# Kernel optimization log

Measured on AMD Instinct MI355X. Metric: run time of the kernel, lower is better.

The kernel has to match this reference:

```python
import jax, jax.numpy as jnp
import numpy as np

B, T, C, H = 8, 1024, 1024, 16
NEG = -1000000000.0
EPS = 1e-12


def setup_inputs() -> dict:
    key = jax.random.key(0)
    ks = jax.random.split(key, 12)
    s = 0.02  # keep pre-softmax logits in a sane range
    return {
        "x": jax.random.normal(ks[0], (B, T, C), jnp.float32),
        "mask": jax.random.randint(ks[1], (B, T), 0, 2, jnp.int32),
        "Wq": jax.random.normal(ks[2], (C, C), jnp.float32) * s,
        "bq": jax.random.normal(ks[3], (C,), jnp.float32) * s,
        "Wk": jax.random.normal(ks[4], (C, C), jnp.float32) * s,
        "bk": jax.random.normal(ks[5], (C,), jnp.float32) * s,
        "Wv": jax.random.normal(ks[6], (C, C), jnp.float32) * s,
        "bv": jax.random.normal(ks[7], (C,), jnp.float32) * s,
        "Wp": jax.random.normal(ks[8], (C, C), jnp.float32) * s,
        "bp": jax.random.normal(ks[9], (C,), jnp.float32) * s,
        "ln_w": jnp.ones((C,), jnp.float32),
        "ln_b": jnp.zeros((C,), jnp.float32),
    }


def reference(x, mask, Wq, bq, Wk, bk, Wv, bv, Wp, bp, ln_w, ln_b):
    Bx, Tx, Cx = x.shape
    hd = Cx // H
    # torch nn.Linear: y = x @ W.T + b
    def lin(inp, W, b):
        return inp @ W.T + b

    def split_heads(t):  # [B,T,C] -> [B,H,T,hd]
        return t.reshape(Bx, Tx, H, hd).transpose(0, 2, 1, 3)

    q = split_heads(lin(x, Wq, bq))
    k = split_heads(lin(x, Wk, bk))
    v = split_heads(lin(x, Wv, bv))

    att = jnp.einsum("bhqd,bhkd->bhqk", q, k) * (1.0 / jnp.sqrt(jnp.float32(hd)))
    # mask [B,T] masks key positions; broadcast to [B,1,1,T]
    att = jnp.where(mask[:, None, None, :] == 0, NEG, att)
    # stable softmax (manual max-subtract, matching original)
    att = jax.nn.softmax(att, axis=-1)
    # dropout prob 0.0 -> identity (eval-mode faithful)
    y = jnp.einsum("bhqk,bhkd->bhqd", att, v)
    y = y.transpose(0, 2, 1, 3).reshape(Bx, Tx, Cx)
    y = lin(y, Wp, bp)
    # residual + LayerNorm(eps=1e-12)
    z = y + x
    mu = jnp.mean(z, axis=-1, keepdims=True)
    var = jnp.mean(jnp.square(z - mu), axis=-1, keepdims=True)
    out = (z - mu) * jax.lax.rsqrt(var + EPS) * ln_w + ln_b
    return out
```

## Files before the change

kernel.cpp:

```cpp
#include <hip/hip_runtime.h>
#include <stdint.h>

#define B_ 8
#define T_ 1024
#define C_ 1024
#define H_ 16
#define HD 64
#define M_TOT (B_ * T_)

using f32x4 = __attribute__((ext_vector_type(4))) float;
using s16x8 = __attribute__((ext_vector_type(8))) short;
using i32x4 = __attribute__((ext_vector_type(4))) int;

__device__ __forceinline__ unsigned short f2bf(float f) {
  unsigned int u = __builtin_bit_cast(unsigned int, f);
  unsigned int r = (u + 0x7fffu + ((u >> 16) & 1u)) >> 16;
  return (unsigned short)r;
}
__device__ __forceinline__ float bf2f(unsigned short s) {
  unsigned int u = ((unsigned int)s) << 16;
  return __builtin_bit_cast(float, u);
}

__device__ __forceinline__ void gload_lds16(const void* g, void* l) {
  __builtin_amdgcn_global_load_lds(
      (const __attribute__((address_space(1))) unsigned int*)g,
      (__attribute__((address_space(3))) unsigned int*)l, 16, 0, 0);
}

__global__ __launch_bounds__(256) void k_convert(
    const float* __restrict__ x, const float* __restrict__ wq,
    const float* __restrict__ wk, const float* __restrict__ wv,
    const float* __restrict__ wp, const float* __restrict__ bq,
    const float* __restrict__ bk, const float* __restrict__ bv,
    const int* __restrict__ maskp, unsigned short* __restrict__ xb,
    unsigned short* __restrict__ wqkv, unsigned short* __restrict__ wpb,
    float* __restrict__ bias_cat, unsigned int* __restrict__ mpair) {
  const long n_x = (long)M_TOT * C_;
  const long W_ELT = (long)C_ * C_;
  const long total4 = (n_x + 4 * W_ELT) >> 2;
  for (long i4 = (long)blockIdx.x * blockDim.x + threadIdx.x; i4 < total4;
       i4 += (long)gridDim.x * blockDim.x) {
    long i = i4 << 2;
    const float* src;
    unsigned short* dst;
    if (i < n_x) {
      src = x + i;
      dst = xb + i;
    } else {
      long off = i - n_x;
      int which = (int)(off >> 20);
      long wo = off & (W_ELT - 1);
      if (which < 3) {
        src = (which == 0 ? wq : which == 1 ? wk : wv) + wo;
        dst = wqkv + which * W_ELT + wo;
      } else {
        src = wp + wo;
        dst = wpb + wo;
      }
    }
    float4 v = *(const float4*)src;
    ushort4 u;
    u.x = f2bf(v.x); u.y = f2bf(v.y); u.z = f2bf(v.z); u.w = f2bf(v.w);
    *(ushort4*)dst = u;
  }
  int t = blockIdx.x * blockDim.x + threadIdx.x;
  if (t < 3 * C_) {
    float v = t < C_ ? bq[t] : (t < 2 * C_ ? bk[t - C_] : bv[t - 2 * C_]);
    bias_cat[t] = v;
  }
  if (t < B_ * T_ / 2) {
    const int* mr = maskp + t * 2;
    mpair[t] = (mr[0] ? 0xFFFFu : 0u) | (mr[1] ? 0xFFFF0000u : 0u);
  }
}

__global__ __launch_bounds__(512, 2) void k_gemm_qkv(
    const unsigned short* __restrict__ A, const unsigned short* __restrict__ Bm,
    const float* __restrict__ bias, unsigned short* __restrict__ q_ws,
    unsigned short* __restrict__ k_ws, unsigned short* __restrict__ vt_ws) {
  __shared__ unsigned short Al[2][256 * 64];
  __shared__ unsigned short Bl[2][256 * 64];
  const int tid = threadIdx.x, lane = tid & 63, w = tid >> 6;
  const int lc = lane & 15, lr = lane >> 4;
  const int wm = w >> 2, wn = w & 3;
  const int GX = 12;
  const int NWG = GX * 32;
  int flat = blockIdx.y * GX + blockIdx.x;
  int swz = (flat & 7) * (NWG / 8) + (flat >> 3);
  const int m0 = (swz / GX) * 256, n0 = (swz % GX) * 256;
  const char* Ab = (const char*)A;
  const char* Bb = (const char*)Bm;

  f32x4 acc[8][4] = {};

  auto stageA = [&](int buf, int kt, int half) {
#pragma unroll
    for (int j = 0; j < 2; ++j) {
      int i = half * 2 + j;
      int g = i * 512 + tid;
      int row = g >> 3, gr = g & 7;
      gload_lds16(Ab + (long)(m0 + row) * 2048 + kt * 128 + ((gr ^ (row & 7)) << 4),
                  (char*)Al[buf] + (long)(i * 512 + w * 64) * 16);
    }
  };
  auto stageB = [&](int buf, int kt, int half) {
#pragma unroll
    for (int j = 0; j < 2; ++j) {
      int i = half * 2 + j;
      int g = i * 512 + tid;
      int row = g >> 3, gr = g & 7;
      gload_lds16(Bb + (long)(n0 + row) * 2048 + kt * 128 + ((gr ^ (row & 7)) << 4),
                  (char*)Bl[buf] + (long)(i * 512 + w * 64) * 16);
    }
  };

  stageA(0, 0, 0);
  stageB(0, 0, 0);
  stageA(0, 0, 1);
  stageB(0, 0, 1);

#pragma unroll
  for (int kt = 0; kt < 16; ++kt) {
    const int cur = kt & 1, nxt = cur ^ 1;
    const bool have = (kt + 1 < 16);
    const char* Ac = (const char*)Al[cur];
    const char* Bc = (const char*)Bl[cur];
    s16x8 aLo[4][2], aHi[4][2], bfr[4][2];

    if (have) stageA(nxt, kt + 1, 0);
    if (have)
      asm volatile("s_waitcnt vmcnt(2)" ::: "memory");
    else
      asm volatile("s_waitcnt vmcnt(0)" ::: "memory");
    __builtin_amdgcn_sched_barrier(0);
    __builtin_amdgcn_s_barrier();
    __builtin_amdgcn_sched_barrier(0);
#pragma unroll
    for (int mf = 0; mf < 4; ++mf) {
      int ar = wm * 128 + mf * 16 + lc;
#pragma unroll
      for (int kk = 0; kk < 2; ++kk)
        aLo[mf][kk] = *(const s16x8*)(Ac + ar * 128 + (((kk * 4 + lr) ^ (ar & 7)) << 4));
    }
#pragma unroll
    for (int nf = 0; nf < 2; ++nf) {
      int br = wn * 64 + nf * 16 + lc;
#pragma unroll
      for (int kk = 0; kk < 2; ++kk)
        bfr[nf][kk] = *(const s16x8*)(Bc + br * 128 + (((kk * 4 + lr) ^ (br & 7)) << 4));
    }
    asm volatile("s_waitcnt lgkmcnt(0)" ::: "memory");
    __builtin_amdgcn_sched_barrier(0);
    __builtin_amdgcn_s_setprio(1);
#pragma unroll
    for (int mf = 0; mf < 4; ++mf)
#pragma unroll
      for (int nf = 0; nf < 2; ++nf)
#pragma unroll
        for (int kk = 0; kk < 2; ++kk)
          acc[mf][nf] = __builtin_amdgcn_mfma_f32_16x16x32_bf16(
              aLo[mf][kk], bfr[nf][kk], acc[mf][nf], 0, 0, 0);
    __builtin_amdgcn_s_setprio(0);

    if (have) stageB(nxt, kt + 1, 0);
#pragma unroll
    for (int nf = 2; nf < 4; ++nf) {
      int br = wn * 64 + nf * 16 + lc;
#pragma unroll
      for (int kk = 0; kk < 2; ++kk)
        bfr[nf][kk] = *(const s16x8*)(Bc + br * 128 + (((kk * 4 + lr) ^ (br & 7)) << 4));
    }
    asm volatile("s_waitcnt lgkmcnt(0)" ::: "memory");
    __builtin_amdgcn_sched_barrier(0);
    __builtin_amdgcn_s_setprio(1);
#pragma unroll
    for (int mf = 0; mf < 4; ++mf)
#pragma unroll
      for (int nf = 2; nf < 4; ++nf)
#pragma unroll
        for (int kk = 0; kk < 2; ++kk)
          acc[mf][nf] = __builtin_amdgcn_mfma_f32_16x16x32_bf16(
              aLo[mf][kk], bfr[nf][kk], acc[mf][nf], 0, 0, 0);
    __builtin_amdgcn_s_setprio(0);

    if (have) stageA(nxt, kt + 1, 1);
#pragma unroll
    for (int mf = 0; mf < 4; ++mf) {
      int ar = wm * 128 + 64 + mf * 16 + lc;
#pragma unroll
      for (int kk = 0; kk < 2; ++kk)
        aHi[mf][kk] = *(const s16x8*)(Ac + ar * 128 + (((kk * 4 + lr) ^ (ar & 7)) << 4));
    }
    asm volatile("s_waitcnt lgkmcnt(0)" ::: "memory");
    __builtin_amdgcn_sched_barrier(0);
    __builtin_amdgcn_s_setprio(1);
#pragma unroll
    for (int mf = 0; mf < 4; ++mf)
#pragma unroll
      for (int nf = 2; nf < 4; ++nf)
#pragma unroll
        for (int kk = 0; kk < 2; ++kk)
          acc[4 + mf][nf] = __builtin_amdgcn_mfma_f32_16x16x32_bf16(
              aHi[mf][kk], bfr[nf][kk], acc[4 + mf][nf], 0, 0, 0);
    __builtin_amdgcn_s_setprio(0);

    if (have) stageB(nxt, kt + 1, 1);
    __builtin_amdgcn_s_setprio(1);
#pragma unroll
    for (int mf = 0; mf < 4; ++mf)
#pragma unroll
      for (int nf = 0; nf < 2; ++nf)
#pragma unroll
        for (int kk = 0; kk < 2; ++kk)
          acc[4 + mf][nf] = __builtin_amdgcn_mfma_f32_16x16x32_bf16(
              aHi[mf][kk], bfr[nf][kk], acc[4 + mf][nf], 0, 0, 0);
    __builtin_amdgcn_s_setprio(0);
    __builtin_amdgcn_sched_barrier(0);
    __builtin_amdgcn_s_barrier();
    __builtin_amdgcn_sched_barrier(0);
  }

#pragma unroll
  for (int mf = 0; mf < 8; ++mf)
#pragma unroll
    for (int nf = 0; nf < 4; ++nf) {
      int gn = n0 + wn * 64 + nf * 16 + lc;
      int which = gn >> 10, nn = gn & 1023;
      int hh = nn >> 6, dd = nn & 63;
      float bia = bias[gn];
      if (which == 2) {
        int gm = m0 + wm * 128 + mf * 16 + lr * 4;
        int bb = gm >> 10, tt = gm & 1023;
        ushort4 pk;
        pk.x = f2bf(acc[mf][nf][0] + bia);
        pk.y = f2bf(acc[mf][nf][1] + bia);
        pk.z = f2bf(acc[mf][nf][2] + bia);
        pk.w = f2bf(acc[mf][nf][3] + bia);
        *(ushort4*)&vt_ws[((long)(bb * H_ + hh) * HD + dd) * T_ + tt] = pk;
      } else {
        unsigned short* dst = (which == 0) ? q_ws : k_ws;
        float scl = (which == 0) ? 0.18033688011112042f : 1.0f;
#pragma unroll
        for (int i = 0; i < 4; ++i) {
          int gm = m0 + wm * 128 + mf * 16 + lr * 4 + i;
          int bb = gm >> 10, tt = gm & 1023;
          dst[((long)(bb * H_ + hh) * T_ + tt) * HD + dd] =
              f2bf((acc[mf][nf][i] + bia) * scl);
        }
      }
    }
}

__global__ __launch_bounds__(256, 2) void k_gemm_proj(
    const unsigned short* __restrict__ A, const unsigned short* __restrict__ Bm,
    const float* __restrict__ bias, const unsigned short* __restrict__ xres16,
    unsigned short* __restrict__ z16) {
  __shared__ unsigned short Al[2][128 * 64];
  __shared__ unsigned short Bl[2][128 * 64];
  const int tid = threadIdx.x, lane = tid & 63, w = tid >> 6;
  const int lc = lane & 15, lr = lane >> 4;
  const int wm = w >> 1, wn = w & 1;
  const int GX = 8;
  const int NWG = GX * 64;
  int flat = blockIdx.y * GX + blockIdx.x;
  int swz = (flat & 7) * (NWG / 8) + (flat >> 3);
  const int m0 = (swz / GX) * 128, n0 = (swz % GX) * 128;
  const char* Ab = (const char*)A;
  const char* Bb = (const char*)Bm;

  f32x4 acc[4][4] = {};

  auto stage = [&](int buf, int kt) {
#pragma unroll
    for (int i = 0; i < 4; ++i) {
      int g = i * 256 + tid;
      int row = g >> 3, gr = g & 7;
      gload_lds16(Ab + (long)(m0 + row) * 2048 + kt * 128 + ((gr ^ (row & 7)) << 4),
                  (char*)Al[buf] + (i * 256 + w * 64) * 16);
    }
#pragma unroll
    for (int i = 0; i < 4; ++i) {
      int g = i * 256 + tid;
      int row = g >> 3, gr = g & 7;
      gload_lds16(Bb + (long)(n0 + row) * 2048 + kt * 128 + ((gr ^ (row & 7)) << 4),
                  (char*)Bl[buf] + (i * 256 + w * 64) * 16);
    }
  };

  stage(0, 0);
  stage(1, 1);
  asm volatile("s_waitcnt vmcnt(8)" ::: "memory");
  __builtin_amdgcn_sched_barrier(0);
  __builtin_amdgcn_s_barrier();
  __builtin_amdgcn_sched_barrier(0);

#pragma unroll
  for (int kt = 0; kt < 16; ++kt) {
    const int cur = kt & 1;
    const char* Ac = (const char*)Al[cur];
    const char* Bc = (const char*)Bl[cur];
    s16x8 af0[4], bf0[4];
#pragma unroll
    for (int mf = 0; mf < 4; ++mf) {
      int ar = wm * 64 + mf * 16 + lc;
      af0[mf] = *(const s16x8*)(Ac + ar * 128 + ((lr ^ (ar & 7)) << 4));
    }
#pragma unroll
    for (int nf = 0; nf < 4; ++nf) {
      int br = wn * 64 + nf * 16 + lc;
      bf0[nf] = *(const s16x8*)(Bc + br * 128 + ((lr ^ (br & 7)) << 4));
    }
#pragma unroll
    for (int mf = 0; mf < 4; ++mf)
#pragma unroll
      for (int nf = 0; nf < 4; ++nf)
        acc[mf][nf] = __builtin_amdgcn_mfma_f32_16x16x32_bf16(af0[mf], bf0[nf],
                                                              acc[mf][nf], 0, 0, 0);
    s16x8 af1[4], bf1[4];
#pragma unroll
    for (int mf = 0; mf < 4; ++mf) {
      int ar = wm * 64 + mf * 16 + lc;
      af1[mf] = *(const s16x8*)(Ac + ar * 128 + (((4 + lr) ^ (ar & 7)) << 4));
    }
#pragma unroll
    for (int nf = 0; nf < 4; ++nf) {
      int br = wn * 64 + nf * 16 + lc;
      bf1[nf] = *(const s16x8*)(Bc + br * 128 + (((4 + lr) ^ (br & 7)) << 4));
    }
    asm volatile("s_waitcnt lgkmcnt(0)" ::: "memory");
    __builtin_amdgcn_sched_barrier(0);
    __builtin_amdgcn_s_barrier();
    __builtin_amdgcn_sched_barrier(0);
    if (kt + 2 < 16) stage(cur, kt + 2);
    __builtin_amdgcn_s_setprio(1);
#pragma unroll
    for (int mf = 0; mf < 4; ++mf)
#pragma unroll
      for (int nf = 0; nf < 4; ++nf)
        acc[mf][nf] = __builtin_amdgcn_mfma_f32_16x16x32_bf16(af1[mf], bf1[nf],
                                                              acc[mf][nf], 0, 0, 0);
    __builtin_amdgcn_s_setprio(0);
    if (kt + 2 < 16)
      asm volatile("s_waitcnt vmcnt(8)" ::: "memory");
    else
      asm volatile("s_waitcnt vmcnt(0)" ::: "memory");
    __builtin_amdgcn_sched_barrier(0);
    __builtin_amdgcn_s_barrier();
    __builtin_amdgcn_sched_barrier(0);
  }

#pragma unroll
  for (int mf = 0; mf < 4; ++mf)
#pragma unroll
    for (int nf = 0; nf < 4; ++nf) {
      int gn = n0 + wn * 64 + nf * 16 + lc;
      float bia = bias[gn];
#pragma unroll
      for (int i = 0; i < 4; ++i) {
        int gm = m0 + wm * 64 + mf * 16 + lr * 4 + i;
        long idx = (long)gm * C_ + gn;
        z16[idx] = f2bf(acc[mf][nf][i] + bia + bf2f(xres16[idx]));
      }
    }
}

__global__ __launch_bounds__(256, 2) void k_attn(
    const unsigned short* __restrict__ Qp, const unsigned short* __restrict__ Kp,
    const unsigned short* __restrict__ Vtp, const unsigned int* __restrict__ mpairp,
    unsigned short* __restrict__ Yp) {
  __shared__ unsigned short Kl[2][64 * 64];
  __shared__ unsigned short Vl[2][64 * 64];
  const int tid = threadIdx.x, lane = tid & 63, w = tid >> 6;
  const int bid = blockIdx.x;
  const int xcd = bid & 7, slot = bid >> 3;
  const int bh = xcd * 16 + (slot >> 2);
  const int qt = slot & 3;
  const int b = bh >> 4, h = bh & 15;
  const int lc = lane & 15, lr = lane >> 4;
  const int q0 = qt * 256 + w * 64;

  const unsigned short* qbase = Qp + ((long)bh * T_ + q0) * HD;
  s16x8 aq[4][2];
#pragma unroll
  for (int g = 0; g < 4; ++g) {
    aq[g][0] = *(const s16x8*)(qbase + (g * 16 + lc) * HD + lr * 8);
    aq[g][1] = *(const s16x8*)(qbase + (g * 16 + lc) * HD + 32 + lr * 8);
  }

  s16x8 ones;
#pragma unroll
  for (int j = 0; j < 8; ++j) ones[j] = (short)0x3F80;

  f32x4 o[4][4] = {};
  f32x4 ol[4] = {};

  const char* kb_g = (const char*)(Kp + (long)bh * T_ * HD);
  const char* vb_g = (const char*)(Vtp + (long)bh * HD * T_);
  const unsigned int* mrow2 = mpairp + b * (T_ / 2);

  auto stage = [&](int buf, int kt) {
#pragma unroll
    for (int it = 0; it < 2; ++it) {
      int f = it * 4096 + w * 1024 + lane * 16;
      int row = f >> 7;
      int swz = (f & 127) ^ ((row & 7) << 4);
      gload_lds16(kb_g + (long)kt * 8192 + (f & ~127) + swz,
                  (char*)Kl[buf] + it * 4096 + w * 1024);
      gload_lds16(vb_g + (long)row * (T_ * 2) + kt * 128 + swz,
                  (char*)Vl[buf] + it * 4096 + w * 1024);
    }
  };

  stage(0, 0);
  __syncthreads();

  const int s01 = lc + ((lane & 16) << 1);
  const int s23 = s01 + 16;
  const bool hi = (lane >= 32);

  int cur = 0;
  for (int kt = 0; kt < T_ / 64; ++kt) {
    if (kt + 1 < T_ / 64) stage(cur ^ 1, kt + 1);

    f32x4 s[4][4];
    const char* kl = (const char*)Kl[cur];
#pragma unroll
    for (int kf = 0; kf < 4; ++kf) {
      int key = kf * 16 + lc;
      s16x8 kb0 = *(const s16x8*)(kl + ((key * 128 + lr * 16) ^ ((key & 7) << 4)));
      s16x8 kb1 = *(const s16x8*)(kl + ((key * 128 + 64 + lr * 16) ^ ((key & 7) << 4)));
#pragma unroll
      for (int g = 0; g < 4; ++g) {
        f32x4 z = {};
        z = __builtin_amdgcn_mfma_f32_16x16x32_bf16(kb0, aq[g][0], z, 0, 0, 0);
        z = __builtin_amdgcn_mfma_f32_16x16x32_bf16(kb1, aq[g][1], z, 0, 0, 0);
        s[g][kf] = z;
      }
    }

    unsigned int mw[4][2];
#pragma unroll
    for (int kf = 0; kf < 4; ++kf) {
      mw[kf][0] = mrow2[kt * 32 + kf * 8 + lr * 2];
      mw[kf][1] = mrow2[kt * 32 + kf * 8 + lr * 2 + 1];
    }

    unsigned int pk[4][4][2];
#pragma unroll
    for (int g = 0; g < 4; ++g)
#pragma unroll
      for (int kf = 0; kf < 4; ++kf) {
        unsigned int u0 = __builtin_bit_cast(unsigned int, __builtin_amdgcn_exp2f(s[g][kf][0]));
        unsigned int u1 = __builtin_bit_cast(unsigned int, __builtin_amdgcn_exp2f(s[g][kf][1]));
        unsigned int u2 = __builtin_bit_cast(unsigned int, __builtin_amdgcn_exp2f(s[g][kf][2]));
        unsigned int u3 = __builtin_bit_cast(unsigned int, __builtin_amdgcn_exp2f(s[g][kf][3]));
        pk[g][kf][0] = ((u1 & 0xFFFF0000u) | (u0 >> 16)) & mw[kf][0];
        pk[g][kf][1] = ((u3 & 0xFFFF0000u) | (u2 >> 16)) & mw[kf][1];
      }

#pragma unroll
    for (int kc = 0; kc < 2; ++kc) {
      s16x8 ap[4];
#pragma unroll
      for (int g = 0; g < 4; ++g) {
        unsigned int A0 = pk[g][kc * 2][0], A1 = pk[g][kc * 2][1];
        unsigned int B0 = pk[g][kc * 2 + 1][0], B1 = pk[g][kc * 2 + 1][1];
        unsigned int w0a = __shfl((int)A0, s01, 64), w0b = __shfl((int)B0, s01, 64);
        unsigned int w1a = __shfl((int)A1, s01, 64), w1b = __shfl((int)B1, s01, 64);
        unsigned int w2a = __shfl((int)A0, s23, 64), w2b = __shfl((int)B0, s23, 64);
        unsigned int w3a = __shfl((int)A1, s23, 64), w3b = __shfl((int)B1, s23, 64);
        i32x4 wv;
        wv[0] = (int)(hi ? w0b : w0a);
        wv[1] = (int)(hi ? w1b : w1a);
        wv[2] = (int)(hi ? w2b : w2a);
        wv[3] = (int)(hi ? w3b : w3a);
        ap[g] = __builtin_bit_cast(s16x8, wv);
      }
      int koff = kc * 64 + lr * 16;
      __builtin_amdgcn_s_setprio(1);
#pragma unroll
      for (int g = 0; g < 4; ++g)
        ol[g] = __builtin_amdgcn_mfma_f32_16x16x32_bf16(ones, ap[g], ol[g], 0, 0, 0);
#pragma unroll
      for (int nf = 0; nf < 4; ++nf) {
        int drow = nf * 16 + lc;
        s16x8 vb = *(const s16x8*)((const char*)Vl[cur] +
                                   ((drow * 128 + koff) ^ ((drow & 7) << 4)));
#pragma unroll
        for (int g = 0; g < 4; ++g)
          o[g][nf] = __builtin_amdgcn_mfma_f32_16x16x32_bf16(vb, ap[g], o[g][nf], 0, 0, 0);
      }
      __builtin_amdgcn_s_setprio(0);
    }
    __syncthreads();
    cur ^= 1;
  }

#pragma unroll
  for (int g = 0; g < 4; ++g) {
    float rl = 1.0f / ol[g][0];
    unsigned short* yrow = Yp + ((long)(b * T_ + q0 + g * 16 + lc)) * C_ + h * 64;
#pragma unroll
    for (int nf = 0; nf < 4; ++nf) {
      ushort4 pw;
      pw.x = f2bf(o[g][nf][0] * rl);
      pw.y = f2bf(o[g][nf][1] * rl);
      pw.z = f2bf(o[g][nf][2] * rl);
      pw.w = f2bf(o[g][nf][3] * rl);
      *(ushort4*)(yrow + nf * 16 + lr * 4) = pw;
    }
  }
}

__global__ __launch_bounds__(256) void k_ln(const unsigned short* __restrict__ z16,
                                            const float* __restrict__ lw,
                                            const float* __restrict__ lb,
                                            float* __restrict__ out) {
  const int row = blockIdx.x;
  ushort4 v16 = ((const ushort4*)(z16 + (long)row * C_))[threadIdx.x];
  float4 v;
  v.x = bf2f(v16.x); v.y = bf2f(v16.y); v.z = bf2f(v16.z); v.w = bf2f(v16.w);
  float s = v.x + v.y + v.z + v.w;
  float s2 = v.x * v.x + v.y * v.y + v.z * v.z + v.w * v.w;
#pragma unroll
  for (int d = 1; d < 64; d <<= 1) {
    s += __shfl_xor(s, d, 64);
    s2 += __shfl_xor(s2, d, 64);
  }
  __shared__ float rs[4], rq[4];
  int wv_ = threadIdx.x >> 6;
  if ((threadIdx.x & 63) == 0) { rs[wv_] = s; rq[wv_] = s2; }
  __syncthreads();
  s = rs[0] + rs[1] + rs[2] + rs[3];
  s2 = rq[0] + rq[1] + rq[2] + rq[3];
  float mu = s * (1.0f / C_);
  float var = s2 * (1.0f / C_) - mu * mu;
  float inv = rsqrtf(var + 1e-12f);
  float4 wv4 = ((const float4*)lw)[threadIdx.x];
  float4 bv4 = ((const float4*)lb)[threadIdx.x];
  float4 ov;
  ov.x = (v.x - mu) * inv * wv4.x + bv4.x;
  ov.y = (v.y - mu) * inv * wv4.y + bv4.y;
  ov.z = (v.z - mu) * inv * wv4.z + bv4.z;
  ov.w = (v.w - mu) * inv * wv4.w + bv4.w;
  ((float4*)(out + (long)row * C_))[threadIdx.x] = ov;
}

extern "C" void kernel_launch(void* const* d_in, const int* in_sizes, int n_in,
                              void* d_out, int out_size, void* d_ws,
                              size_t ws_size, hipStream_t stream) {
  const float* x = (const float*)d_in[0];
  const int* mask = (const int*)d_in[1];
  const float* Wq = (const float*)d_in[2];
  const float* bq = (const float*)d_in[3];
  const float* Wk = (const float*)d_in[4];
  const float* bk = (const float*)d_in[5];
  const float* Wv = (const float*)d_in[6];
  const float* bv = (const float*)d_in[7];
  const float* Wp = (const float*)d_in[8];
  const float* bp = (const float*)d_in[9];
  const float* lnw = (const float*)d_in[10];
  const float* lnb = (const float*)d_in[11];
  float* out = (float*)d_out;

  char* ws = (char*)d_ws;
  const size_t MB = 1024 * 1024;
  unsigned short* xb = (unsigned short*)(ws);
  unsigned short* q_ws = (unsigned short*)(ws + 16 * MB);
  unsigned short* k_ws = (unsigned short*)(ws + 32 * MB);
  unsigned short* vt_ws = (unsigned short*)(ws + 48 * MB);
  unsigned short* y_ws = (unsigned short*)(ws + 64 * MB);
  unsigned short* wqkv = (unsigned short*)(ws + 80 * MB);
  unsigned short* wpb = (unsigned short*)(ws + 86 * MB);
  float* bias_cat = (float*)(ws + 88 * MB);
  unsigned int* mpair = (unsigned int*)(ws + 88 * MB + 16384);
  unsigned short* z16 = (unsigned short*)(ws + 48 * MB);

  k_convert<<<dim3(2048), dim3(256), 0, stream>>>(x, Wq, Wk, Wv, Wp, bq, bk, bv,
                                                  mask, xb, wqkv, wpb, bias_cat,
                                                  mpair);
  k_gemm_qkv<<<dim3(12, 32), dim3(512), 0, stream>>>(xb, wqkv, bias_cat, q_ws,
                                                     k_ws, vt_ws);
  k_attn<<<dim3(512), dim3(256), 0, stream>>>(q_ws, k_ws, vt_ws, mpair, y_ws);
  k_gemm_proj<<<dim3(8, 64), dim3(256), 0, stream>>>(y_ws, wpb, bp, xb, z16);
  k_ln<<<dim3(8192), dim3(256), 0, stream>>>(z16, lnw, lnb, out);
}
```

Before: 174.5 us.

## Restructure QKV GEMM main loop to prefetch two k-tiles ahead

Replaces the interleaved half-tile staging of A and B with a two-stage prefetch. Both LDS buffers are filled up front, and each buffer is refilled two iterations ahead once its fragments have been read into registers. Each k-tile is now split into two k-halves, each loading all A and B fragments before its MFMAs. This is meant to hide global-load latency over a whole iteration and cut waitcnt stalls, at the cost of more live fragment registers and coarser compute/load interleaving.

```diff
diff --git a/kernel.cpp b/kernel.cpp
--- a/kernel.cpp
+++ b/kernel.cpp
@@ -94,20 +94,16 @@
 
   f32x4 acc[8][4] = {};
 
-  auto stageA = [&](int buf, int kt, int half) {
-#pragma unroll
-    for (int j = 0; j < 2; ++j) {
-      int i = half * 2 + j;
+  auto stage = [&](int buf, int kt) {
+#pragma unroll
+    for (int i = 0; i < 4; ++i) {
       int g = i * 512 + tid;
       int row = g >> 3, gr = g & 7;
       gload_lds16(Ab + (long)(m0 + row) * 2048 + kt * 128 + ((gr ^ (row & 7)) << 4),
                   (char*)Al[buf] + (long)(i * 512 + w * 64) * 16);
     }
-  };
-  auto stageB = [&](int buf, int kt, int half) {
-#pragma unroll
-    for (int j = 0; j < 2; ++j) {
-      int i = half * 2 + j;
+#pragma unroll
+    for (int i = 0; i < 4; ++i) {
       int g = i * 512 + tid;
       int row = g >> 3, gr = g & 7;
       gload_lds16(Bb + (long)(n0 + row) * 2048 + kt * 128 + ((gr ^ (row & 7)) << 4),
@@ -115,107 +111,63 @@
     }
   };
 
-  stageA(0, 0, 0);
-  stageB(0, 0, 0);
-  stageA(0, 0, 1);
-  stageB(0, 0, 1);
+  stage(0, 0);
+  stage(1, 1);
+  asm volatile("s_waitcnt vmcnt(8)" ::: "memory");
+  __builtin_amdgcn_sched_barrier(0);
+  __builtin_amdgcn_s_barrier();
+  __builtin_amdgcn_sched_barrier(0);
 
 #pragma unroll
   for (int kt = 0; kt < 16; ++kt) {
-    const int cur = kt & 1, nxt = cur ^ 1;
-    const bool have = (kt + 1 < 16);
+    const int cur = kt & 1;
     const char* Ac = (const char*)Al[cur];
     const char* Bc = (const char*)Bl[cur];
-    s16x8 aLo[4][2], aHi[4][2], bfr[4][2];
-
-    if (have) stageA(nxt, kt + 1, 0);
-    if (have)
-      asm volatile("s_waitcnt vmcnt(2)" ::: "memory");
+    s16x8 af0[8], bf0[4];
+#pragma unroll
+    for (int mf = 0; mf < 8; ++mf) {
+      int ar = wm * 128 + mf * 16 + lc;
+      af0[mf] = *(const s16x8*)(Ac + ar * 128 + ((lr ^ (ar & 7)) << 4));
+    }
+#pragma unroll
+    for (int nf = 0; nf < 4; ++nf) {
+      int br = wn * 64 + nf * 16 + lc;
+      bf0[nf] = *(const s16x8*)(Bc + br * 128 + ((lr ^ (br & 7)) << 4));
+    }
+#pragma unroll
+    for (int mf = 0; mf < 8; ++mf)
+#pragma unroll
+      for (int nf = 0; nf < 4; ++nf)
+        acc[mf][nf] = __builtin_amdgcn_mfma_f32_16x16x32_bf16(af0[mf], bf0[nf],
+                                                              acc[mf][nf], 0, 0, 0);
+    s16x8 af1[8], bf1[4];
+#pragma unroll
+    for (int mf = 0; mf < 8; ++mf) {
+      int ar = wm * 128 + mf * 16 + lc;
+      af1[mf] = *(const s16x8*)(Ac + ar * 128 + (((4 + lr) ^ (ar & 7)) << 4));
+    }
+#pragma unroll
+    for (int nf = 0; nf < 4; ++nf) {
+      int br = wn * 64 + nf * 16 + lc;
+      bf1[nf] = *(const s16x8*)(Bc + br * 128 + (((4 + lr) ^ (br & 7)) << 4));
+    }
+    asm volatile("s_waitcnt lgkmcnt(0)" ::: "memory");
+    __builtin_amdgcn_sched_barrier(0);
+    __builtin_amdgcn_s_barrier();
+    __builtin_amdgcn_sched_barrier(0);
+    if (kt + 2 < 16) stage(cur, kt + 2);
+    __builtin_amdgcn_s_setprio(1);
+#pragma unroll
+    for (int mf = 0; mf < 8; ++mf)
+#pragma unroll
+      for (int nf = 0; nf < 4; ++nf)
+        acc[mf][nf] = __builtin_amdgcn_mfma_f32_16x16x32_bf16(af1[mf], bf1[nf],
+                                                              acc[mf][nf], 0, 0, 0);
+    __builtin_amdgcn_s_setprio(0);
+    if (kt + 2 < 16)
+      asm volatile("s_waitcnt vmcnt(8)" ::: "memory");
     else
       asm volatile("s_waitcnt vmcnt(0)" ::: "memory");
-    __builtin_amdgcn_sched_barrier(0);
-    __builtin_amdgcn_s_barrier();
-    __builtin_amdgcn_sched_barrier(0);
-#pragma unroll
-    for (int mf = 0; mf < 4; ++mf) {
-      int ar = wm * 128 + mf * 16 + lc;
-#pragma unroll
-      for (int kk = 0; kk < 2; ++kk)
-        aLo[mf][kk] = *(const s16x8*)(Ac + ar * 128 + (((kk * 4 + lr) ^ (ar & 7)) << 4));
-    }
-#pragma unroll
-    for (int nf = 0; nf < 2; ++nf) {
-      int br = wn * 64 + nf * 16 + lc;
-#pragma unroll
-      for (int kk = 0; kk < 2; ++kk)
-        bfr[nf][kk] = *(const s16x8*)(Bc + br * 128 + (((kk * 4 + lr) ^ (br & 7)) << 4));
-    }
-    asm volatile("s_waitcnt lgkmcnt(0)" ::: "memory");
-    __builtin_amdgcn_sched_barrier(0);
-    __builtin_amdgcn_s_setprio(1);
-#pragma unroll
-    for (int mf = 0; mf < 4; ++mf)
-#pragma unroll
-      for (int nf = 0; nf < 2; ++nf)
-#pragma unroll
-        for (int kk = 0; kk < 2; ++kk)
-          acc[mf][nf] = __builtin_amdgcn_mfma_f32_16x16x32_bf16(
-              aLo[mf][kk], bfr[nf][kk], acc[mf][nf], 0, 0, 0);
-    __builtin_amdgcn_s_setprio(0);
-
-    if (have) stageB(nxt, kt + 1, 0);
-#pragma unroll
-    for (int nf = 2; nf < 4; ++nf) {
-      int br = wn * 64 + nf * 16 + lc;
-#pragma unroll
-      for (int kk = 0; kk < 2; ++kk)
-        bfr[nf][kk] = *(const s16x8*)(Bc + br * 128 + (((kk * 4 + lr) ^ (br & 7)) << 4));
-    }
-    asm volatile("s_waitcnt lgkmcnt(0)" ::: "memory");
-    __builtin_amdgcn_sched_barrier(0);
-    __builtin_amdgcn_s_setprio(1);
-#pragma unroll
-    for (int mf = 0; mf < 4; ++mf)
-#pragma unroll
-      for (int nf = 2; nf < 4; ++nf)
-#pragma unroll
-        for (int kk = 0; kk < 2; ++kk)
-          acc[mf][nf] = __builtin_amdgcn_mfma_f32_16x16x32_bf16(
-              aLo[mf][kk], bfr[nf][kk], acc[mf][nf], 0, 0, 0);
-    __builtin_amdgcn_s_setprio(0);
-
-    if (have) stageA(nxt, kt + 1, 1);
-#pragma unroll
-    for (int mf = 0; mf < 4; ++mf) {
-      int ar = wm * 128 + 64 + mf * 16 + lc;
-#pragma unroll
-      for (int kk = 0; kk < 2; ++kk)
-        aHi[mf][kk] = *(const s16x8*)(Ac + ar * 128 + (((kk * 4 + lr) ^ (ar & 7)) << 4));
-    }
-    asm volatile("s_waitcnt lgkmcnt(0)" ::: "memory");
-    __builtin_amdgcn_sched_barrier(0);
-    __builtin_amdgcn_s_setprio(1);
-#pragma unroll
-    for (int mf = 0; mf < 4; ++mf)
-#pragma unroll
-      for (int nf = 2; nf < 4; ++nf)
-#pragma unroll
-        for (int kk = 0; kk < 2; ++kk)
-          acc[4 + mf][nf] = __builtin_amdgcn_mfma_f32_16x16x32_bf16(
-              aHi[mf][kk], bfr[nf][kk], acc[4 + mf][nf], 0, 0, 0);
-    __builtin_amdgcn_s_setprio(0);
-
-    if (have) stageB(nxt, kt + 1, 1);
-    __builtin_amdgcn_s_setprio(1);
-#pragma unroll
-    for (int mf = 0; mf < 4; ++mf)
-#pragma unroll
-      for (int nf = 0; nf < 2; ++nf)
-#pragma unroll
-        for (int kk = 0; kk < 2; ++kk)
-          acc[4 + mf][nf] = __builtin_amdgcn_mfma_f32_16x16x32_bf16(
-              aHi[mf][kk], bfr[nf][kk], acc[4 + mf][nf], 0, 0, 0);
-    __builtin_amdgcn_s_setprio(0);
     __builtin_amdgcn_sched_barrier(0);
     __builtin_amdgcn_s_barrier();
     __builtin_amdgcn_sched_barrier(0);
```

After: 167.9 us. -3.8%, faster.
